# Performance work log

Measured on AMD Instinct MI355X. Metric: run time of the kernel, lower is better.

Reference implementation:

```python
import jax, jax.numpy as jnp
import numpy as np

T, B, H, L = 512, 32, 512, 2  # seq_len, batch, hidden_size, num_layers (input_size == H)


def _lstm_layer(x, Wih, Whh, bih, bhh):
    """x: [T,B,D]; Wih: [4H,D]; Whh: [4H,H]; biases: [4H]. Returns [T,B,H]."""
    # Precompute input contribution for all timesteps (one big GEMM).
    x_proj = jnp.einsum('tbd,gd->tbg', x, Wih) + bih + bhh  # [T,B,4H]
    h0 = jnp.zeros((x.shape[1], H), x.dtype)
    c0 = jnp.zeros((x.shape[1], H), x.dtype)

    def step(carry, xp):
        h, c = carry
        z = xp + h @ Whh.T  # [B,4H]
        i = jax.nn.sigmoid(z[:, 0 * H:1 * H])
        f = jax.nn.sigmoid(z[:, 1 * H:2 * H])
        g = jnp.tanh(z[:, 2 * H:3 * H])
        o = jax.nn.sigmoid(z[:, 3 * H:4 * H])
        c_new = f * c + i * g
        h_new = o * jnp.tanh(c_new)
        return (h_new, c_new), h_new

    (_, _), ys = jax.lax.scan(step, (h0, c0), x_proj)
    return ys  # [T,B,H]


def setup_inputs() -> dict:
    key = jax.random.key(0)
    k1, k2, k3, k4, k5 = jax.random.split(key, 5)
    scale = 1.0 / np.sqrt(H)  # torch Linear default init range ~ U(-1/sqrt(fan_in), ...)
    return {
        'seq_inputs': jax.random.normal(k1, (T, B, H), jnp.float32),
        'W_ih': jax.random.normal(k2, (L, 4 * H, H), jnp.float32) * scale,
        'W_hh': jax.random.normal(k3, (L, 4 * H, H), jnp.float32) * scale,
        'b_ih': jax.random.normal(k4, (L, 4 * H), jnp.float32) * scale,
        'b_hh': jax.random.normal(k5, (L, 4 * H), jnp.float32) * scale,
    }


def reference(seq_inputs, W_ih, W_hh, b_ih, b_hh):
    x = seq_inputs
    for l in range(L):  # small fixed layer loop
        x = _lstm_layer(x, W_ih[l], W_hh[l], b_ih[l], b_hh[l])
    return x  # [T,B,H] last-layer hidden sequence
```

## Files before the change

### kernel.cpp

```cpp
#include <hip/hip_runtime.h>


typedef _Float16 half8_t __attribute__((ext_vector_type(8)));
typedef _Float16 half4_t __attribute__((ext_vector_type(4)));
typedef float f32x4 __attribute__((ext_vector_type(4)));
typedef unsigned int u32;
typedef unsigned short u16;

#define T_LEN 512
#define BATCH 32
#define HID 512
#define SLOT 16384
#define LW (2048 * 512)

__device__ __forceinline__ float fast_sigmoid(float x) {
  return 1.f / (1.f + __expf(-x));
}
__device__ __forceinline__ float fast_tanh(float x) {
  return 1.f - 2.f / (1.f + __expf(2.f * x));
}

__global__ __launch_bounds__(256) void convert_k(
    const float4* __restrict__ x,
    const float4* __restrict__ wih,
    const float4* __restrict__ whh,
    const float* __restrict__ bih, const float* __restrict__ bhh,
    half4_t* __restrict__ xh, half4_t* __restrict__ wihh, half4_t* __restrict__ whhh,
    float* __restrict__ bsum) {
  const int N4X = 2097152, N4W = 524288, TOT = N4X + 2 * N4W;
  int gid = blockIdx.x * 256 + threadIdx.x;
  for (int i = gid; i < TOT; i += gridDim.x * 256) {
    float4 v;
    half4_t* dst;
    if (i < N4X) { v = x[i]; dst = xh + i; }
    else if (i < N4X + N4W) { v = wih[i - N4X]; dst = wihh + (i - N4X); }
    else { v = whh[i - N4X - N4W]; dst = whhh + (i - N4X - N4W); }
    half4_t h;
    h[0] = (_Float16)v.x; h[1] = (_Float16)v.y; h[2] = (_Float16)v.z; h[3] = (_Float16)v.w;
    *dst = h;
  }
  if (gid < 4096) bsum[gid] = bih[gid] + bhh[gid];
}

__global__ __launch_bounds__(128, 1) void lstm_fused(
    const _Float16* __restrict__ x0h,
    const _Float16* __restrict__ wih16,
    const _Float16* __restrict__ whh16,
    const float* __restrict__ bsum,
    _Float16* h0seq,
    _Float16* h1seq,
    u32* flags0, u32* flags1,
    float* outf) {
  int bid = blockIdx.x;
  int layer = bid >> 6, wg = bid & 63;
  int tid = threadIdx.x;
  int ln = tid & 63;
  int q = ln >> 4, l15 = ln & 15;
  int m0 = (tid >> 6) * 16;

  const _Float16* wih_l = wih16 + (size_t)layer * LW;
  const _Float16* whh_l = whh16 + (size_t)layer * LW;
  half8_t wx[2][16], wh[2][16];
  float bv[2];
#pragma unroll
  for (int j = 0; j < 2; ++j) {
    int nl = j * 16 + l15;
    int grow = (nl >> 3) * 512 + wg * 8 + (nl & 7);
    size_t ro = (size_t)grow * 512;
#pragma unroll
    for (int kc = 0; kc < 16; ++kc) {
      wx[j][kc] = *(const half8_t*)(wih_l + ro + kc * 32 + q * 8);
      wh[j][kc] = *(const half8_t*)(whh_l + ro + kc * 32 + q * 8);
    }
    bv[j] = bsum[layer * 2048 + grow];
  }

  const _Float16* xbase = layer ? (h0seq + SLOT) : x0h;
  _Float16* hself = layer ? h1seq : h0seq;
  u32* fself = layer ? flags1 : flags0;

  int cb = tid >> 2;
  int cp = tid & 3;
  int col0 = wg * 8 + cp * 2;
  float cst0 = 0.f, cst1 = 0.f;

  __shared__ float Zs[4 * 297];

  for (int t = 1; t <= T_LEN; ++t) {
    const _Float16* xsrc = xbase + (size_t)(t - 1) * SLOT;
    const _Float16* hsrc = hself + (size_t)(t - 1) * SLOT;
    f32x4 acc0 = {}, acc1 = {};
    half8_t af[16];

    if (layer == 0) {
#pragma unroll
      for (int kc = 0; kc < 16; ++kc)
        af[kc] = *(const half8_t*)(xsrc + (m0 + l15) * HID + kc * 32 + q * 8);
#pragma unroll
      for (int kc = 0; kc < 16; ++kc) {
        acc0 = __builtin_amdgcn_mfma_f32_16x16x32_f16(af[kc], wx[0][kc], acc0, 0, 0, 0);
        acc1 = __builtin_amdgcn_mfma_f32_16x16x32_f16(af[kc], wx[1][kc], acc1, 0, 0, 0);
      }
      u32 tgt = (u32)(t - 1);
      while (__hip_atomic_load(&fself[ln], __ATOMIC_RELAXED, __HIP_MEMORY_SCOPE_AGENT) < tgt) {
        __builtin_amdgcn_s_sleep(1);
      }
      asm volatile("" ::: "memory");
    } else {
      u32 tgt = (u32)t;
      while (__hip_atomic_load(&flags0[ln], __ATOMIC_RELAXED, __HIP_MEMORY_SCOPE_AGENT) < tgt) {
        __builtin_amdgcn_s_sleep(1);
      }
      asm volatile("" ::: "memory");
#pragma unroll
      for (int kc = 0; kc < 16; ++kc)
        af[kc] = *(const half8_t*)(xsrc + (m0 + l15) * HID + kc * 32 + q * 8);
#pragma unroll
      for (int kc = 0; kc < 16; ++kc) {
        acc0 = __builtin_amdgcn_mfma_f32_16x16x32_f16(af[kc], wx[0][kc], acc0, 0, 0, 0);
        acc1 = __builtin_amdgcn_mfma_f32_16x16x32_f16(af[kc], wx[1][kc], acc1, 0, 0, 0);
      }
      u32 tgt1 = (u32)(t - 1);
      while (__hip_atomic_load(&flags1[ln], __ATOMIC_RELAXED, __HIP_MEMORY_SCOPE_AGENT) < tgt1) {
        __builtin_amdgcn_s_sleep(1);
      }
      asm volatile("" ::: "memory");
    }

#pragma unroll
    for (int kc = 0; kc < 16; ++kc)
      af[kc] = *(const half8_t*)(hsrc + (m0 + l15) * HID + kc * 32 + q * 8);
#pragma unroll
    for (int kc = 0; kc < 16; ++kc) {
      acc0 = __builtin_amdgcn_mfma_f32_16x16x32_f16(af[kc], wh[0][kc], acc0, 0, 0, 0);
      acc1 = __builtin_amdgcn_mfma_f32_16x16x32_f16(af[kc], wh[1][kc], acc1, 0, 0, 0);
    }

#pragma unroll
    for (int j = 0; j < 2; ++j) {
      int nl = j * 16 + l15, g = nl >> 3, c = nl & 7;
      const f32x4& a = j ? acc1 : acc0;
#pragma unroll
      for (int r = 0; r < 4; ++r)
        Zs[g * 297 + (m0 + q * 4 + r) * 9 + c] = a[r] + bv[j];
    }
    __syncthreads();

    {
      float zi0 = Zs[0 * 297 + cb * 9 + cp * 2], zi1 = Zs[0 * 297 + cb * 9 + cp * 2 + 1];
      float zf0 = Zs[1 * 297 + cb * 9 + cp * 2], zf1 = Zs[1 * 297 + cb * 9 + cp * 2 + 1];
      float zg0 = Zs[2 * 297 + cb * 9 + cp * 2], zg1 = Zs[2 * 297 + cb * 9 + cp * 2 + 1];
      float zo0 = Zs[3 * 297 + cb * 9 + cp * 2], zo1 = Zs[3 * 297 + cb * 9 + cp * 2 + 1];
      float i0 = fast_sigmoid(zi0), f0 = fast_sigmoid(zf0), g0 = fast_tanh(zg0), o0 = fast_sigmoid(zo0);
      float i1 = fast_sigmoid(zi1), f1 = fast_sigmoid(zf1), g1 = fast_tanh(zg1), o1 = fast_sigmoid(zo1);
      cst0 = f0 * cst0 + i0 * g0;
      cst1 = f1 * cst1 + i1 * g1;
      float h0 = o0 * fast_tanh(cst0);
      float h1 = o1 * fast_tanh(cst1);
      u32 hp = (u32)__builtin_bit_cast(u16, (_Float16)h0) |
               ((u32)__builtin_bit_cast(u16, (_Float16)h1) << 16);
      u32* hdst = (u32*)(hself + (size_t)t * SLOT + cb * HID + col0);
      __hip_atomic_store(hdst, hp, __ATOMIC_RELAXED, __HIP_MEMORY_SCOPE_AGENT);
      if (layer) {
        float2 o2; o2.x = h0; o2.y = h1;
        *(float2*)(outf + (size_t)(t - 1) * SLOT + cb * HID + col0) = o2;
      }
    }
    __syncthreads();
    if (tid == 0)
      __hip_atomic_store(&fself[wg], (u32)t, __ATOMIC_RELAXED, __HIP_MEMORY_SCOPE_AGENT);
  }
}

extern "C" void kernel_launch(void* const* d_in, const int* in_sizes, int n_in,
                              void* d_out, int out_size, void* d_ws, size_t ws_size,
                              hipStream_t stream) {
  const float* x = (const float*)d_in[0];
  const float* Wih = (const float*)d_in[1];
  const float* Whh = (const float*)d_in[2];
  const float* bih = (const float*)d_in[3];
  const float* bhh = (const float*)d_in[4];
  char* ws = (char*)d_ws;
  const size_t OFF_X0H = 0;
  const size_t OFF_H0SEQ = 16777216;
  const size_t OFF_H1SEQ = 33587200;
  const size_t OFF_WIH = 50397184;
  const size_t OFF_WHH = 54591488;
  const size_t OFF_BSUM = 58785792;
  const size_t OFF_FLAGS0 = 58802176;
  const size_t OFF_FLAGS1 = 58802432;
  const size_t TOTAL = 58802688;
  if (ws_size < TOTAL) return;
  _Float16* x0h = (_Float16*)(ws + OFF_X0H);
  _Float16* h0seq = (_Float16*)(ws + OFF_H0SEQ);
  _Float16* h1seq = (_Float16*)(ws + OFF_H1SEQ);
  _Float16* wihh = (_Float16*)(ws + OFF_WIH);
  _Float16* whhh = (_Float16*)(ws + OFF_WHH);
  float* bsum = (float*)(ws + OFF_BSUM);
  u32* flags0 = (u32*)(ws + OFF_FLAGS0);
  u32* flags1 = (u32*)(ws + OFF_FLAGS1);

  hipMemsetAsync(ws + OFF_FLAGS0, 0, 512, stream);
  hipMemsetAsync(ws + OFF_H0SEQ, 0, 32768, stream);
  hipMemsetAsync(ws + OFF_H1SEQ, 0, 32768, stream);
  convert_k<<<3072, 256, 0, stream>>>((const float4*)x, (const float4*)Wih,
                                      (const float4*)Whh, bih, bhh,
                                      (half4_t*)x0h, (half4_t*)wihh, (half4_t*)whhh, bsum);
  lstm_fused<<<128, 128, 0, stream>>>(x0h, wihh, whhh, bsum, h0seq, h1seq,
                                      flags0, flags1, (float*)d_out);
}
```

Baseline: 3.698 ms.

## Replace per-workgroup flag array with single atomic epoch counter per layer

Each layer's 64 workgroups now signal step completion by atomically incrementing one shared epoch counter, replacing per-workgroup flag stores. Waiters poll a single address for 64*t instead of each lane polling its own flag. Layer 1 now waits on both layers' counters in one combined loop before its input projection, where it previously waited on its own recurrence after that projection. The fp32 output store is moved after the signal so it leaves the critical path. Many workgroups contending on one atomic address could add latency in exchange for cheaper polling.

```diff
diff --git a/kernel.cpp b/kernel.cpp
--- a/kernel.cpp
+++ b/kernel.cpp
@@ -18,6 +18,9 @@
 }
 __device__ __forceinline__ float fast_tanh(float x) {
   return 1.f - 2.f / (1.f + __expf(2.f * x));
+}
+__device__ __forceinline__ u32 epoch_peek(const u32* p) {
+  return __hip_atomic_load(p, __ATOMIC_RELAXED, __HIP_MEMORY_SCOPE_AGENT);
 }
 
 __global__ __launch_bounds__(256) void convert_k(
@@ -49,7 +52,7 @@
     const float* __restrict__ bsum,
     _Float16* h0seq,
     _Float16* h1seq,
-    u32* flags0, u32* flags1,
+    u32* epoch0, u32* epoch1,
     float* outf) {
   int bid = blockIdx.x;
   int layer = bid >> 6, wg = bid & 63;
@@ -77,7 +80,7 @@
 
   const _Float16* xbase = layer ? (h0seq + SLOT) : x0h;
   _Float16* hself = layer ? h1seq : h0seq;
-  u32* fself = layer ? flags1 : flags0;
+  u32* eself = layer ? epoch1 : epoch0;
 
   int cb = tid >> 2;
   int cp = tid & 3;
@@ -101,14 +104,12 @@
         acc0 = __builtin_amdgcn_mfma_f32_16x16x32_f16(af[kc], wx[0][kc], acc0, 0, 0, 0);
         acc1 = __builtin_amdgcn_mfma_f32_16x16x32_f16(af[kc], wx[1][kc], acc1, 0, 0, 0);
       }
-      u32 tgt = (u32)(t - 1);
-      while (__hip_atomic_load(&fself[ln], __ATOMIC_RELAXED, __HIP_MEMORY_SCOPE_AGENT) < tgt) {
-        __builtin_amdgcn_s_sleep(1);
-      }
+      u32 tgt = 64u * (u32)(t - 1);
+      while (epoch_peek(epoch0) < tgt) { __builtin_amdgcn_s_sleep(1); }
       asm volatile("" ::: "memory");
     } else {
-      u32 tgt = (u32)t;
-      while (__hip_atomic_load(&flags0[ln], __ATOMIC_RELAXED, __HIP_MEMORY_SCOPE_AGENT) < tgt) {
+      u32 tgt0 = 64u * (u32)t, tgt1 = 64u * (u32)(t - 1);
+      while (epoch_peek(epoch0) < tgt0 || epoch_peek(epoch1) < tgt1) {
         __builtin_amdgcn_s_sleep(1);
       }
       asm volatile("" ::: "memory");
@@ -120,11 +121,6 @@
         acc0 = __builtin_amdgcn_mfma_f32_16x16x32_f16(af[kc], wx[0][kc], acc0, 0, 0, 0);
         acc1 = __builtin_amdgcn_mfma_f32_16x16x32_f16(af[kc], wx[1][kc], acc1, 0, 0, 0);
       }
-      u32 tgt1 = (u32)(t - 1);
-      while (__hip_atomic_load(&flags1[ln], __ATOMIC_RELAXED, __HIP_MEMORY_SCOPE_AGENT) < tgt1) {
-        __builtin_amdgcn_s_sleep(1);
-      }
-      asm volatile("" ::: "memory");
     }
 
 #pragma unroll
@@ -146,6 +142,7 @@
     }
     __syncthreads();
 
+    float h0, h1;
     {
       float zi0 = Zs[0 * 297 + cb * 9 + cp * 2], zi1 = Zs[0 * 297 + cb * 9 + cp * 2 + 1];
       float zf0 = Zs[1 * 297 + cb * 9 + cp * 2], zf1 = Zs[1 * 297 + cb * 9 + cp * 2 + 1];
@@ -155,20 +152,20 @@
       float i1 = fast_sigmoid(zi1), f1 = fast_sigmoid(zf1), g1 = fast_tanh(zg1), o1 = fast_sigmoid(zo1);
       cst0 = f0 * cst0 + i0 * g0;
       cst1 = f1 * cst1 + i1 * g1;
-      float h0 = o0 * fast_tanh(cst0);
-      float h1 = o1 * fast_tanh(cst1);
+      h0 = o0 * fast_tanh(cst0);
+      h1 = o1 * fast_tanh(cst1);
       u32 hp = (u32)__builtin_bit_cast(u16, (_Float16)h0) |
                ((u32)__builtin_bit_cast(u16, (_Float16)h1) << 16);
       u32* hdst = (u32*)(hself + (size_t)t * SLOT + cb * HID + col0);
       __hip_atomic_store(hdst, hp, __ATOMIC_RELAXED, __HIP_MEMORY_SCOPE_AGENT);
-      if (layer) {
-        float2 o2; o2.x = h0; o2.y = h1;
-        *(float2*)(outf + (size_t)(t - 1) * SLOT + cb * HID + col0) = o2;
-      }
     }
     __syncthreads();
     if (tid == 0)
-      __hip_atomic_store(&fself[wg], (u32)t, __ATOMIC_RELAXED, __HIP_MEMORY_SCOPE_AGENT);
+      (void)__hip_atomic_fetch_add(eself, 1u, __ATOMIC_RELAXED, __HIP_MEMORY_SCOPE_AGENT);
+    if (layer) {
+      float2 o2; o2.x = h0; o2.y = h1;
+      *(float2*)(outf + (size_t)(t - 1) * SLOT + cb * HID + col0) = o2;
+    }
   }
 }
 
@@ -187,8 +184,8 @@
   const size_t OFF_WIH = 50397184;
   const size_t OFF_WHH = 54591488;
   const size_t OFF_BSUM = 58785792;
-  const size_t OFF_FLAGS0 = 58802176;
-  const size_t OFF_FLAGS1 = 58802432;
+  const size_t OFF_EPOCH0 = 58802176;
+  const size_t OFF_EPOCH1 = 58802432;
   const size_t TOTAL = 58802688;
   if (ws_size < TOTAL) return;
   _Float16* x0h = (_Float16*)(ws + OFF_X0H);
@@ -197,15 +194,15 @@
   _Float16* wihh = (_Float16*)(ws + OFF_WIH);
   _Float16* whhh = (_Float16*)(ws + OFF_WHH);
   float* bsum = (float*)(ws + OFF_BSUM);
-  u32* flags0 = (u32*)(ws + OFF_FLAGS0);
-  u32* flags1 = (u32*)(ws + OFF_FLAGS1);
-
-  hipMemsetAsync(ws + OFF_FLAGS0, 0, 512, stream);
+  u32* epoch0 = (u32*)(ws + OFF_EPOCH0);
+  u32* epoch1 = (u32*)(ws + OFF_EPOCH1);
+
+  hipMemsetAsync(ws + OFF_EPOCH0, 0, 512, stream);
   hipMemsetAsync(ws + OFF_H0SEQ, 0, 32768, stream);
   hipMemsetAsync(ws + OFF_H1SEQ, 0, 32768, stream);
   convert_k<<<3072, 256, 0, stream>>>((const float4*)x, (const float4*)Wih,
                                       (const float4*)Whh, bih, bhh,
                                       (half4_t*)x0h, (half4_t*)wihh, (half4_t*)whhh, bsum);
   lstm_fused<<<128, 128, 0, stream>>>(x0h, wihh, whhh, bsum, h0seq, h1seq,
-                                      flags0, flags1, (float*)d_out);
-}
+                                      epoch0, epoch1, (float*)d_out);
+}
```

Measured after the change: 3.388 ms. 8.4% less time.
